# Kernel tuning notes

Hardware: AMD Instinct MI355X
Metric: run time of the kernel (lower is better)

The kernel has to match this reference:

```python
import jax, jax.numpy as jnp
import numpy as np

V, D, H, T, L, B = 32000, 1024, 16, 1024, 2, 2
HD = D // H
FF = 4 * D
EPS_RMS = 1.1920929e-07  # torch.finfo(float32).eps (RMSNorm default eps=None)
EPS_LN = 1e-5


def _rope_diag():
    # Faithful to the torch code: theta = 10000.0 ** (-2*i) // head_size
    # (** binds tighter than //), which is 0.0 for all i when head_size > 1,
    # and the einsum 'bimm,bim->bim' only reads the diagonal of the rotation
    # matrix, whose entries are cos((c+1)*theta).
    k = np.arange(0, HD, 2, dtype=np.float64)
    theta = (10000.0 ** (-2.0 * k)) // HD          # [HD//2], all zeros
    pos = np.arange(1, T + 1, dtype=np.float64)[:, None]
    cosv = np.cos(pos * theta)                      # [T, HD//2]
    diag = np.repeat(cosv, 2, axis=1)               # [T, HD]
    return jnp.asarray(diag, dtype=jnp.float32)


def setup_inputs() -> dict:
    key = jax.random.key(0)
    ks = jax.random.split(key, 12)
    s = 0.02
    n = lambda k, shape: jax.random.normal(k, shape, jnp.float32) * s
    return dict(
        idx=jax.random.randint(ks[0], (B, T), 0, V),
        emb=n(ks[1], (V, D)),
        wq=n(ks[2], (L, H, D, HD)),
        wk=n(ks[3], (L, H, D, HD)),
        wv=n(ks[4], (L, H, D, HD)),
        attn_w=n(ks[5], (L, D, D)),
        attn_b=jnp.zeros((L, D), jnp.float32),
        n1_w=jnp.ones((L, D), jnp.float32),
        n2_w=jnp.ones((L, D), jnp.float32),
        f1_w=n(ks[6], (L, D, FF)),
        f1_b=jnp.zeros((L, FF), jnp.float32),
        fs_w=n(ks[7], (L, FF, FF)),
        fs_b=jnp.zeros((L, FF), jnp.float32),
        f2_w=n(ks[8], (L, FF, D)),
        f2_b=jnp.zeros((L, D), jnp.float32),
        ln_w=jnp.ones((D,), jnp.float32),
        ln_b=jnp.zeros((D,), jnp.float32),
        out_w=n(ks[9], (D, V)),
        out_b=jnp.zeros((V,), jnp.float32),
    )


def _rmsnorm(x, w):
    return x * jax.lax.rsqrt(jnp.mean(x * x, axis=-1, keepdims=True) + EPS_RMS) * w


def _layernorm(x, w, b):
    mu = jnp.mean(x, axis=-1, keepdims=True)
    var = jnp.mean((x - mu) ** 2, axis=-1, keepdims=True)
    return (x - mu) * jax.lax.rsqrt(var + EPS_LN) * w + b


def _forward(idx, emb, wq, wk, wv, attn_w, attn_b, n1_w, n2_w,
             f1_w, f1_b, fs_w, fs_b, f2_w, f2_b, ln_w, ln_b, out_w, out_b):
    rope = _rope_diag()                              # [T, HD]
    mask = jnp.tril(jnp.ones((T, T), dtype=bool))    # causal
    scale = 1.0 / np.sqrt(HD)
    x = emb[idx]                                     # [B, T, D]
    for l in range(L):
        h = _rmsnorm(x, n1_w[l])
        q = jnp.einsum('btd,hdk->bhtk', h, wq[l])
        k = jnp.einsum('btd,hdk->bhtk', h, wk[l]) * rope[None, None]
        v = jnp.einsum('btd,hdk->bhtk', h, wv[l])
        score = jnp.einsum('bhtk,bhsk->bhts', q, k) * scale
        score = jnp.where(mask, score, -jnp.inf)
        att = jax.nn.softmax(score, axis=-1)
        o = jnp.einsum('bhts,bhsk->bhtk', att, v)
        o = o.transpose(0, 2, 1, 3).reshape(B, T, D)  # concat heads
        x = x + (o @ attn_w[l] + attn_b[l])
        h = _rmsnorm(x, n2_w[l])
        a = h @ f1_w[l] + f1_b[l]
        g = a @ fs_w[l] + fs_b[l]                     # fcswiglu applied to fc1 output
        x = x + (jax.nn.silu(a) * g) @ f2_w[l] + f2_b[l]
    x = _layernorm(x, ln_w, ln_b)
    return x @ out_w + out_b                          # [B, T, V]


def reference(idx, emb, wq, wk, wv, attn_w, attn_b, n1_w, n2_w,
              f1_w, f1_b, fs_w, fs_b, f2_w, f2_b, ln_w, ln_b, out_w, out_b):
    return _forward(idx, emb, wq, wk, wv, attn_w, attn_b, n1_w, n2_w,
                    f1_w, f1_b, fs_w, fs_b, f2_w, f2_b, ln_w, ln_b, out_w, out_b)
```

## Files before the change

### kernel.cpp

```cpp
#include <hip/hip_runtime.h>

#define BB   2
#define TT   1024
#define HH   16
#define DD   1024
#define HDD  64
#define FFD  4096
#define VV   32000
#define LLAY 2

typedef __bf16 bf16x8 __attribute__((ext_vector_type(8)));
typedef float  f32x4  __attribute__((ext_vector_type(4)));
typedef unsigned short u16x8 __attribute__((ext_vector_type(8)));

__device__ __forceinline__ float bf2f(ushort u) {
    return __uint_as_float(((unsigned int)u) << 16);
}
__device__ __forceinline__ ushort f2bf(float f) {
    unsigned int u = __float_as_uint(f);
    u += 0x7fffu + ((u >> 16) & 1u);
    return (ushort)(u >> 16);
}

__device__ __forceinline__ void gl_lds16(const ushort* g, ushort* l) {
    typedef const __attribute__((address_space(1))) unsigned int* gp_t;
    typedef __attribute__((address_space(3))) unsigned int* lp_t;
    __builtin_amdgcn_global_load_lds((gp_t)g, (lp_t)l, 16, 0, 0);
}

__global__ void embed_k(const int* __restrict__ idx, const float* __restrict__ emb,
                        float* __restrict__ x) {
    int row = blockIdx.x, tid = threadIdx.x;
    int e = idx[row];
    float4 f = *(const float4*)(emb + (size_t)e * DD + tid * 4);
    *(float4*)(x + (size_t)row * DD + tid * 4) = f;
}

__global__ __launch_bounds__(256) void rmsnorm_k(const float* __restrict__ x,
                                                 const float* __restrict__ w,
                                                 ushort* __restrict__ h) {
    int row = blockIdx.x, tid = threadIdx.x;
    int wave = tid >> 6, lane = tid & 63;
    const float* xr = x + (size_t)row * DD;
    float4 xv = *(const float4*)(xr + tid * 4);
    float s = xv.x * xv.x + xv.y * xv.y + xv.z * xv.z + xv.w * xv.w;
    for (int off = 32; off; off >>= 1) s += __shfl_xor(s, off, 64);
    __shared__ float red[4];
    if (lane == 0) red[wave] = s;
    __syncthreads();
    float tot = red[0] + red[1] + red[2] + red[3];
    float rs = rsqrtf(tot * (1.0f / DD) + 1.1920929e-07f);
    float4 wv = *(const float4*)(w + tid * 4);
    ushort4 hv;
    hv.x = f2bf(xv.x * rs * wv.x);
    hv.y = f2bf(xv.y * rs * wv.y);
    hv.z = f2bf(xv.z * rs * wv.z);
    hv.w = f2bf(xv.w * rs * wv.w);
    *(ushort4*)(h + (size_t)row * DD + tid * 4) = hv;
}

__global__ __launch_bounds__(256) void lnorm_k(const float* __restrict__ x,
                                               const float* __restrict__ w,
                                               const float* __restrict__ b,
                                               ushort* __restrict__ h) {
    int row = blockIdx.x, tid = threadIdx.x;
    int wave = tid >> 6, lane = tid & 63;
    const float* xr = x + (size_t)row * DD;
    float4 xv = *(const float4*)(xr + tid * 4);
    float s1 = xv.x + xv.y + xv.z + xv.w;
    for (int off = 32; off; off >>= 1) s1 += __shfl_xor(s1, off, 64);
    __shared__ float r1[4], r2[4];
    if (lane == 0) r1[wave] = s1;
    __syncthreads();
    float mu = (r1[0] + r1[1] + r1[2] + r1[3]) * (1.0f / DD);
    float dx0 = xv.x - mu, dx1 = xv.y - mu, dx2 = xv.z - mu, dx3 = xv.w - mu;
    float s2 = dx0 * dx0 + dx1 * dx1 + dx2 * dx2 + dx3 * dx3;
    for (int off = 32; off; off >>= 1) s2 += __shfl_xor(s2, off, 64);
    if (lane == 0) r2[wave] = s2;
    __syncthreads();
    float var = (r2[0] + r2[1] + r2[2] + r2[3]) * (1.0f / DD);
    float rs = rsqrtf(var + 1e-5f);
    float4 wv = *(const float4*)(w + tid * 4);
    float4 bv = *(const float4*)(b + tid * 4);
    ushort4 hv;
    hv.x = f2bf(dx0 * rs * wv.x + bv.x);
    hv.y = f2bf(dx1 * rs * wv.y + bv.y);
    hv.z = f2bf(dx2 * rs * wv.z + bv.z);
    hv.w = f2bf(dx3 * rs * wv.w + bv.w);
    *(ushort4*)(h + (size_t)row * DD + tid * 4) = hv;
}

__global__ void silu_k(ushort* __restrict__ a, const ushort* __restrict__ g) {
    int i = (blockIdx.x * 256 + threadIdx.x) * 4;
    ushort4 av = *(const ushort4*)(a + i);
    ushort4 gv = *(const ushort4*)(g + i);
    ushort4 ov;
    {
        float x = bf2f(av.x); ov.x = f2bf(x / (1.0f + __expf(-x)) * bf2f(gv.x));
        float y = bf2f(av.y); ov.y = f2bf(y / (1.0f + __expf(-y)) * bf2f(gv.y));
        float z = bf2f(av.z); ov.z = f2bf(z / (1.0f + __expf(-z)) * bf2f(gv.z));
        float u = bf2f(av.w); ov.w = f2bf(u / (1.0f + __expf(-u)) * bf2f(gv.w));
    }
    *(ushort4*)(a + i) = ov;
}

__global__ __launch_bounds__(256) void transp_k(const float* __restrict__ in,
                                                ushort* __restrict__ out,
                                                int K, int N,
                                                long long inB, long long outB) {
    __shared__ int tbuf[64][65];
    const float* ip = in + (size_t)blockIdx.z * inB;
    ushort* op = out + (size_t)blockIdx.z * outB;
    int n0 = blockIdx.x * 64, k0 = blockIdx.y * 64;
    int tid = threadIdx.x;
#pragma unroll
    for (int jj = 0; jj < 4; ++jj) {
        int idxq = tid + jj * 256;
        int rr = idxq >> 4;
        int cc = (idxq & 15) * 4;
        float4 f = *(const float4*)(ip + (size_t)(k0 + rr) * N + n0 + cc);
        tbuf[rr][cc]     = f2bf(f.x);
        tbuf[rr][cc + 1] = f2bf(f.y);
        tbuf[rr][cc + 2] = f2bf(f.z);
        tbuf[rr][cc + 3] = f2bf(f.w);
    }
    __syncthreads();
#pragma unroll
    for (int jj = 0; jj < 4; ++jj) {
        int idxq = tid + jj * 256;
        int rr = idxq >> 4;
        int cc = (idxq & 15) * 4;
        ushort4 v;
        v.x = (ushort)tbuf[cc][rr];
        v.y = (ushort)tbuf[cc + 1][rr];
        v.z = (ushort)tbuf[cc + 2][rr];
        v.w = (ushort)tbuf[cc + 3][rr];
        *(ushort4*)(op + (size_t)(n0 + rr) * K + k0 + cc) = v;
    }
}

template <bool BIAS, bool RESID, bool OUTBF>
__global__ __launch_bounds__(256) void gemm_k(const ushort* __restrict__ A,
                                              const ushort* __restrict__ Bt,
                                              const float* __restrict__ bias,
                                              const float* __restrict__ resid,
                                              void* __restrict__ Cout,
                                              int M, int N, int K) {
    __shared__ __align__(16) ushort As[2][128 * 32];
    __shared__ __align__(16) ushort Bs[2][128 * 32];
    const int tid = threadIdx.x;
    const int m0 = blockIdx.y * 128, n0 = blockIdx.x * 128;
    const int wave = tid >> 6, lane = tid & 63;
    const int waveM = (wave >> 1) * 64, waveN = (wave & 1) * 64;
    const int lrow = lane & 15, quad = lane >> 4;

    const int srow = wave * 32 + (lane >> 2);
    const int scol = (lane & 3) * 8;
    const ushort* pa = A + (size_t)(m0 + srow) * K + scol;
    const ushort* pb = Bt + (size_t)(n0 + srow) * K + scol;
    ushort* lA = &As[0][0] + wave * 32 * 32;
    ushort* lB = &Bs[0][0] + wave * 32 * 32;

    f32x4 acc[4][4];
    f32x4 zero = {0.f, 0.f, 0.f, 0.f};
#pragma unroll
    for (int i = 0; i < 4; i++)
#pragma unroll
        for (int j = 0; j < 4; j++) acc[i][j] = zero;

    const int nk = K >> 5;

#define STAGE(buf, kt)                                                         \
    do {                                                                       \
        const ushort* ga = pa + (size_t)(kt) * 32;                             \
        const ushort* gb = pb + (size_t)(kt) * 32;                             \
        ushort* la = lA + (size_t)(buf) * 128 * 32;                            \
        ushort* lb = lB + (size_t)(buf) * 128 * 32;                            \
        gl_lds16(ga, la);                                                      \
        gl_lds16(ga + (size_t)16 * K, la + 16 * 32);                           \
        gl_lds16(gb, lb);                                                      \
        gl_lds16(gb + (size_t)16 * K, lb + 16 * 32);                           \
    } while (0)

    STAGE(0, 0);
    int cur = 0;
    for (int kt = 0; kt < nk; ++kt) {
        __syncthreads();
        if (kt + 1 < nk) STAGE(cur ^ 1, kt + 1);
        bf16x8 af[4], bfr[4];
#pragma unroll
        for (int i = 0; i < 4; i++)
            af[i] = *(const bf16x8*)&As[cur][(waveM + i * 16 + lrow) * 32 + quad * 8];
#pragma unroll
        for (int j = 0; j < 4; j++)
            bfr[j] = *(const bf16x8*)&Bs[cur][(waveN + j * 16 + lrow) * 32 + quad * 8];
#pragma unroll
        for (int i = 0; i < 4; i++)
#pragma unroll
            for (int j = 0; j < 4; j++)
                acc[i][j] = __builtin_amdgcn_mfma_f32_16x16x32_bf16(af[i], bfr[j], acc[i][j], 0, 0, 0);
        cur ^= 1;
    }
#undef STAGE

#pragma unroll
    for (int i = 0; i < 4; i++) {
#pragma unroll
        for (int j = 0; j < 4; j++) {
            int colg = n0 + waveN + j * 16 + lrow;
            float bv = BIAS ? bias[colg] : 0.f;
#pragma unroll
            for (int rr = 0; rr < 4; ++rr) {
                int rowg = m0 + waveM + i * 16 + quad * 4 + rr;
                size_t off = (size_t)rowg * N + colg;
                float vv = acc[i][j][rr] + bv;
                if (RESID) vv += resid[off];
                if (OUTBF) ((ushort*)Cout)[off] = f2bf(vv);
                else       ((float*)Cout)[off] = vv;
            }
        }
    }
}

__global__ __launch_bounds__(128) void attn_k(const ushort* __restrict__ qkv,
                                              ushort* __restrict__ o) {
    __shared__ __align__(16) ushort vt[64 * 80];
    __shared__ __align__(16) ushort pl[2 * 16 * 80];
    const int bid = blockIdx.x;
    const int bh = bid & 31;
    const int qt = 31 - (bid >> 5);
    const int b = bh >> 4, h = bh & 15;
    const int t0 = qt * 32;
    const int tid = threadIdx.x, wave = tid >> 6, lane = tid & 63;
    const int lrow = lane & 15, quad = lane >> 4;
    const int LD3 = 3 * DD;
    const size_t base3 = (size_t)(b * TT) * LD3 + (size_t)h * HDD;
    const int t0w = t0 + wave * 16;

    const ushort* qrow = qkv + base3 + (size_t)(t0w + lrow) * LD3 + quad * 8;
    bf16x8 af0 = *(const bf16x8*)(qrow);
    bf16x8 af1 = *(const bf16x8*)(qrow + 32);

    f32x4 acc_o[4];
    f32x4 zero = {0.f, 0.f, 0.f, 0.f};
#pragma unroll
    for (int n = 0; n < 4; ++n) acc_o[n] = zero;
    float m_r[4], l_r[4];
#pragma unroll
    for (int r = 0; r < 4; ++r) { m_r[r] = -1e30f; l_r[r] = 0.f; }

    ushort* plw = pl + wave * 16 * 80;

    const int smax = t0 + 31;
    for (int s0 = 0; s0 <= smax; s0 += 64) {
        __syncthreads();
        bf16x8 bk[4][2];
#pragma unroll
        for (int j = 0; j < 4; ++j) {
            const ushort* kr = qkv + base3 + (size_t)(s0 + j * 16 + lrow) * LD3 + DD + quad * 8;
            bk[j][0] = *(const bf16x8*)(kr);
            bk[j][1] = *(const bf16x8*)(kr + 32);
        }
#pragma unroll
        for (int cc = 0; cc < 4; ++cc) {
            int qch = tid + cc * 128;
            int s = qch & 63, d0 = (qch >> 6) * 8;
            u16x8 vv = *(const u16x8*)(qkv + base3 + (size_t)(s0 + s) * LD3 + 2 * DD + d0);
#pragma unroll
            for (int i = 0; i < 8; ++i) vt[(d0 + i) * 80 + s] = vv[i];
        }
        f32x4 accs[4];
#pragma unroll
        for (int j = 0; j < 4; ++j) {
            accs[j] = zero;
            accs[j] = __builtin_amdgcn_mfma_f32_16x16x32_bf16(af0, bk[j][0], accs[j], 0, 0, 0);
            accs[j] = __builtin_amdgcn_mfma_f32_16x16x32_bf16(af1, bk[j][1], accs[j], 0, 0, 0);
        }
        float pv[4][4];
#pragma unroll
        for (int r = 0; r < 4; ++r) {
            int qg = t0w + quad * 4 + r;
            float scv[4], tmax = -1e30f;
#pragma unroll
            for (int j = 0; j < 4; ++j) {
                int sg = s0 + j * 16 + lrow;
                float sc = (sg <= qg) ? accs[j][r] * 0.125f : -1e30f;
                scv[j] = sc;
                tmax = fmaxf(tmax, sc);
            }
            tmax = fmaxf(tmax, __shfl_xor(tmax, 1, 64));
            tmax = fmaxf(tmax, __shfl_xor(tmax, 2, 64));
            tmax = fmaxf(tmax, __shfl_xor(tmax, 4, 64));
            tmax = fmaxf(tmax, __shfl_xor(tmax, 8, 64));
            float mn = fmaxf(m_r[r], tmax);
            float ps = 0.f;
#pragma unroll
            for (int j = 0; j < 4; ++j) {
                float p = __expf(scv[j] - mn);
                pv[j][r] = p;
                ps += p;
            }
            ps += __shfl_xor(ps, 1, 64);
            ps += __shfl_xor(ps, 2, 64);
            ps += __shfl_xor(ps, 4, 64);
            ps += __shfl_xor(ps, 8, 64);
            float alpha = __expf(m_r[r] - mn);
            l_r[r] = l_r[r] * alpha + ps;
            m_r[r] = mn;
#pragma unroll
            for (int n = 0; n < 4; ++n) acc_o[n][r] *= alpha;
        }
#pragma unroll
        for (int j = 0; j < 4; ++j)
#pragma unroll
            for (int r = 0; r < 4; ++r)
                plw[(quad * 4 + r) * 80 + j * 16 + lrow] = f2bf(pv[j][r]);
        __syncthreads();
        bf16x8 pa0 = *(const bf16x8*)&plw[lrow * 80 + quad * 8];
        bf16x8 pa1 = *(const bf16x8*)&plw[lrow * 80 + 32 + quad * 8];
#pragma unroll
        for (int n = 0; n < 4; ++n) {
            bf16x8 bv0 = *(const bf16x8*)&vt[(n * 16 + lrow) * 80 + quad * 8];
            bf16x8 bv1 = *(const bf16x8*)&vt[(n * 16 + lrow) * 80 + 32 + quad * 8];
            acc_o[n] = __builtin_amdgcn_mfma_f32_16x16x32_bf16(pa0, bv0, acc_o[n], 0, 0, 0);
            acc_o[n] = __builtin_amdgcn_mfma_f32_16x16x32_bf16(pa1, bv1, acc_o[n], 0, 0, 0);
        }
    }
#pragma unroll
    for (int n = 0; n < 4; ++n)
#pragma unroll
        for (int r = 0; r < 4; ++r) {
            int tg = t0w + quad * 4 + r;
            o[(size_t)(b * TT + tg) * DD + h * HDD + n * 16 + lrow] = f2bf(acc_o[n][r] / l_r[r]);
        }
}

extern "C" void kernel_launch(void* const* d_in, const int* in_sizes, int n_in,
                              void* d_out, int out_size, void* d_ws, size_t ws_size,
                              hipStream_t stream) {
    const int*   idx    = (const int*)d_in[0];
    const float* emb    = (const float*)d_in[1];
    const float* wq     = (const float*)d_in[2];
    const float* wk     = (const float*)d_in[3];
    const float* wvv    = (const float*)d_in[4];
    const float* attn_w = (const float*)d_in[5];
    const float* attn_b = (const float*)d_in[6];
    const float* n1_w   = (const float*)d_in[7];
    const float* n2_w   = (const float*)d_in[8];
    const float* f1_w   = (const float*)d_in[9];
    const float* f1_b   = (const float*)d_in[10];
    const float* fs_w   = (const float*)d_in[11];
    const float* fs_b   = (const float*)d_in[12];
    const float* f2_w   = (const float*)d_in[13];
    const float* f2_b   = (const float*)d_in[14];
    const float* ln_w   = (const float*)d_in[15];
    const float* ln_b   = (const float*)d_in[16];
    const float* out_w  = (const float*)d_in[17];
    const float* out_b  = (const float*)d_in[18];

    const int BT = BB * TT;

    char* ws = (char*)d_ws;
    size_t off = 0;
    float* x = (float*)(ws + off);          off += (size_t)BT * DD * 4;
    ushort* wpack = (ushort*)(ws + off);    off += (size_t)VV * DD * 2;
    ushort* h = (ushort*)(ws + off);        off += (size_t)BT * DD * 2;
    ushort* qkv = (ushort*)(ws + off);      off += (size_t)BT * 3 * DD * 2;
    ushort* ob = (ushort*)(ws + off);       off += (size_t)BT * DD * 2;
    ushort* a = (ushort*)(ws + off);        off += (size_t)BT * FFD * 2;
    ushort* g = (ushort*)(ws + off);        off += (size_t)BT * FFD * 2;

    ushort* qkvT = wpack;
    ushort* attnT = wpack + (size_t)3 * DD * DD;
    ushort* f1T  = attnT + (size_t)DD * DD;
    ushort* fsT  = f1T + (size_t)FFD * DD;
    ushort* f2T  = fsT + (size_t)FFD * FFD;

    dim3 blk(256);

    embed_k<<<BT, blk, 0, stream>>>(idx, emb, x);

    for (int l = 0; l < LLAY; ++l) {
        const size_t woff_qkv = (size_t)l * HH * DD * HDD;
        transp_k<<<dim3(1, 16, 16), blk, 0, stream>>>(wq + woff_qkv, qkvT, DD, HDD,
                                                      (long long)DD * HDD, (long long)HDD * DD);
        transp_k<<<dim3(1, 16, 16), blk, 0, stream>>>(wk + woff_qkv, qkvT + (size_t)DD * DD, DD, HDD,
                                                      (long long)DD * HDD, (long long)HDD * DD);
        transp_k<<<dim3(1, 16, 16), blk, 0, stream>>>(wvv + woff_qkv, qkvT + (size_t)2 * DD * DD, DD, HDD,
                                                      (long long)DD * HDD, (long long)HDD * DD);
        transp_k<<<dim3(16, 16, 1), blk, 0, stream>>>(attn_w + (size_t)l * DD * DD, attnT, DD, DD, 0, 0);
        transp_k<<<dim3(64, 16, 1), blk, 0, stream>>>(f1_w + (size_t)l * DD * FFD, f1T, DD, FFD, 0, 0);
        transp_k<<<dim3(64, 64, 1), blk, 0, stream>>>(fs_w + (size_t)l * FFD * FFD, fsT, FFD, FFD, 0, 0);
        transp_k<<<dim3(16, 64, 1), blk, 0, stream>>>(f2_w + (size_t)l * FFD * DD, f2T, FFD, DD, 0, 0);

        rmsnorm_k<<<BT, blk, 0, stream>>>(x, n1_w + l * DD, h);
        gemm_k<false, false, true><<<dim3(24, 16), blk, 0, stream>>>(h, qkvT, nullptr, nullptr, qkv,
                                                                     BT, 3 * DD, DD);
        attn_k<<<BB * HH * (TT / 32), dim3(128), 0, stream>>>(qkv, ob);
        gemm_k<true, true, false><<<dim3(8, 16), blk, 0, stream>>>(ob, attnT, attn_b + l * DD, x, x,
                                                                   BT, DD, DD);
        rmsnorm_k<<<BT, blk, 0, stream>>>(x, n2_w + l * DD, h);
        gemm_k<true, false, true><<<dim3(32, 16), blk, 0, stream>>>(h, f1T, f1_b + l * FFD, nullptr, a,
                                                                    BT, FFD, DD);
        gemm_k<true, false, true><<<dim3(32, 16), blk, 0, stream>>>(a, fsT, fs_b + l * FFD, nullptr, g,
                                                                    BT, FFD, FFD);
        silu_k<<<(BT * FFD) / 1024, blk, 0, stream>>>(a, g);
        gemm_k<true, true, false><<<dim3(8, 16), blk, 0, stream>>>(a, f2T, f2_b + l * DD, x, x,
                                                                   BT, DD, FFD);
    }

    lnorm_k<<<BT, blk, 0, stream>>>(x, ln_w, ln_b, h);
    transp_k<<<dim3(500, 16, 1), blk, 0, stream>>>(out_w, wpack, DD, VV, 0, 0);
    gemm_k<true, false, false><<<dim3(250, 16), blk, 0, stream>>>(h, wpack, out_b, nullptr,
                                                                  (float*)d_out, BT, VV, DD);
}
```

Before: 1.408 ms.

## Triple-buffer GEMM loads, fuse SiLU gate into fs GEMM epilogue, nontemporal logits

The GEMM k-loop moves from double to triple buffering in LDS. It waits with explicit vmcnt counts and a single barrier per iteration, so global-to-LDS loads run two tiles ahead of the MFMA work. The standalone SiLU kernel is removed and silu(a)*g is computed in the epilogue of the fcswiglu GEMM, reading a as an auxiliary input. The final logits GEMM writes its fp32 output with nontemporal stores. The costs are more LDS per block, which may lower occupancy, and the hand-written waitcnt/barrier logic, which depends on the exact number of outstanding loads.

```diff
diff --git a/kernel.cpp b/kernel.cpp
--- a/kernel.cpp
+++ b/kernel.cpp
@@ -90,20 +90,6 @@
     *(ushort4*)(h + (size_t)row * DD + tid * 4) = hv;
 }
 
-__global__ void silu_k(ushort* __restrict__ a, const ushort* __restrict__ g) {
-    int i = (blockIdx.x * 256 + threadIdx.x) * 4;
-    ushort4 av = *(const ushort4*)(a + i);
-    ushort4 gv = *(const ushort4*)(g + i);
-    ushort4 ov;
-    {
-        float x = bf2f(av.x); ov.x = f2bf(x / (1.0f + __expf(-x)) * bf2f(gv.x));
-        float y = bf2f(av.y); ov.y = f2bf(y / (1.0f + __expf(-y)) * bf2f(gv.y));
-        float z = bf2f(av.z); ov.z = f2bf(z / (1.0f + __expf(-z)) * bf2f(gv.z));
-        float u = bf2f(av.w); ov.w = f2bf(u / (1.0f + __expf(-u)) * bf2f(gv.w));
-    }
-    *(ushort4*)(a + i) = ov;
-}
-
 __global__ __launch_bounds__(256) void transp_k(const float* __restrict__ in,
                                                 ushort* __restrict__ out,
                                                 int K, int N,
@@ -139,15 +125,15 @@
     }
 }
 
-template <bool BIAS, bool RESID, bool OUTBF>
+template <bool BIAS, int EPI, bool OUTBF, bool NT>
 __global__ __launch_bounds__(256) void gemm_k(const ushort* __restrict__ A,
                                               const ushort* __restrict__ Bt,
                                               const float* __restrict__ bias,
-                                              const float* __restrict__ resid,
+                                              const void* __restrict__ aux,
                                               void* __restrict__ Cout,
                                               int M, int N, int K) {
-    __shared__ __align__(16) ushort As[2][128 * 32];
-    __shared__ __align__(16) ushort Bs[2][128 * 32];
+    __shared__ __align__(16) ushort As[3][128 * 32];
+    __shared__ __align__(16) ushort Bs[3][128 * 32];
     const int tid = threadIdx.x;
     const int m0 = blockIdx.y * 128, n0 = blockIdx.x * 128;
     const int wave = tid >> 6, lane = tid & 63;
@@ -183,23 +169,26 @@
     } while (0)
 
     STAGE(0, 0);
-    int cur = 0;
+    if (nk > 1) STAGE(1, 1);
     for (int kt = 0; kt < nk; ++kt) {
-        __syncthreads();
-        if (kt + 1 < nk) STAGE(cur ^ 1, kt + 1);
+        if (kt + 1 < nk) asm volatile("s_waitcnt vmcnt(4)" ::: "memory");
+        else             asm volatile("s_waitcnt vmcnt(0)" ::: "memory");
+        __builtin_amdgcn_s_barrier();
+        __builtin_amdgcn_sched_barrier(0);
+        if (kt + 2 < nk) STAGE((kt + 2) % 3, kt + 2);
+        const int sl = kt % 3;
         bf16x8 af[4], bfr[4];
 #pragma unroll
         for (int i = 0; i < 4; i++)
-            af[i] = *(const bf16x8*)&As[cur][(waveM + i * 16 + lrow) * 32 + quad * 8];
+            af[i] = *(const bf16x8*)&As[sl][(waveM + i * 16 + lrow) * 32 + quad * 8];
 #pragma unroll
         for (int j = 0; j < 4; j++)
-            bfr[j] = *(const bf16x8*)&Bs[cur][(waveN + j * 16 + lrow) * 32 + quad * 8];
+            bfr[j] = *(const bf16x8*)&Bs[sl][(waveN + j * 16 + lrow) * 32 + quad * 8];
 #pragma unroll
         for (int i = 0; i < 4; i++)
 #pragma unroll
             for (int j = 0; j < 4; j++)
                 acc[i][j] = __builtin_amdgcn_mfma_f32_16x16x32_bf16(af[i], bfr[j], acc[i][j], 0, 0, 0);
-        cur ^= 1;
     }
 #undef STAGE
 
@@ -214,9 +203,14 @@
                 int rowg = m0 + waveM + i * 16 + quad * 4 + rr;
                 size_t off = (size_t)rowg * N + colg;
                 float vv = acc[i][j][rr] + bv;
-                if (RESID) vv += resid[off];
+                if (EPI == 1) vv += ((const float*)aux)[off];
+                if (EPI == 2) {
+                    float s = bf2f(((const ushort*)aux)[off]);
+                    vv *= s / (1.0f + __expf(-s));
+                }
                 if (OUTBF) ((ushort*)Cout)[off] = f2bf(vv);
-                else       ((float*)Cout)[off] = vv;
+                else if (NT) __builtin_nontemporal_store(vv, (float*)Cout + off);
+                else ((float*)Cout)[off] = vv;
             }
         }
     }
@@ -394,23 +388,22 @@
         transp_k<<<dim3(16, 64, 1), blk, 0, stream>>>(f2_w + (size_t)l * FFD * DD, f2T, FFD, DD, 0, 0);
 
         rmsnorm_k<<<BT, blk, 0, stream>>>(x, n1_w + l * DD, h);
-        gemm_k<false, false, true><<<dim3(24, 16), blk, 0, stream>>>(h, qkvT, nullptr, nullptr, qkv,
-                                                                     BT, 3 * DD, DD);
+        gemm_k<false, 0, true, false><<<dim3(24, 16), blk, 0, stream>>>(h, qkvT, nullptr, nullptr, qkv,
+                                                                        BT, 3 * DD, DD);
         attn_k<<<BB * HH * (TT / 32), dim3(128), 0, stream>>>(qkv, ob);
-        gemm_k<true, true, false><<<dim3(8, 16), blk, 0, stream>>>(ob, attnT, attn_b + l * DD, x, x,
-                                                                   BT, DD, DD);
+        gemm_k<true, 1, false, false><<<dim3(8, 16), blk, 0, stream>>>(ob, attnT, attn_b + l * DD, x, x,
+                                                                       BT, DD, DD);
         rmsnorm_k<<<BT, blk, 0, stream>>>(x, n2_w + l * DD, h);
-        gemm_k<true, false, true><<<dim3(32, 16), blk, 0, stream>>>(h, f1T, f1_b + l * FFD, nullptr, a,
-                                                                    BT, FFD, DD);
-        gemm_k<true, false, true><<<dim3(32, 16), blk, 0, stream>>>(a, fsT, fs_b + l * FFD, nullptr, g,
-                                                                    BT, FFD, FFD);
-        silu_k<<<(BT * FFD) / 1024, blk, 0, stream>>>(a, g);
-        gemm_k<true, true, false><<<dim3(8, 16), blk, 0, stream>>>(a, f2T, f2_b + l * DD, x, x,
-                                                                   BT, DD, FFD);
+        gemm_k<true, 0, true, false><<<dim3(32, 16), blk, 0, stream>>>(h, f1T, f1_b + l * FFD, nullptr, a,
+                                                                       BT, FFD, DD);
+        gemm_k<true, 2, true, false><<<dim3(32, 16), blk, 0, stream>>>(a, fsT, fs_b + l * FFD, a, g,
+                                                                       BT, FFD, FFD);
+        gemm_k<true, 1, false, false><<<dim3(8, 16), blk, 0, stream>>>(g, f2T, f2_b + l * DD, x, x,
+                                                                       BT, DD, FFD);
     }
 
     lnorm_k<<<BT, blk, 0, stream>>>(x, ln_w, ln_b, h);
     transp_k<<<dim3(500, 16, 1), blk, 0, stream>>>(out_w, wpack, DD, VV, 0, 0);
-    gemm_k<true, false, false><<<dim3(250, 16), blk, 0, stream>>>(h, wpack, out_b, nullptr,
-                                                                  (float*)d_out, BT, VV, DD);
-}
+    gemm_k<true, 0, false, true><<<dim3(250, 16), blk, 0, stream>>>(h, wpack, out_b, nullptr,
+                                                                    (float*)d_out, BT, VV, DD);
+}
```

Result: no change. 1.430 ms (+1.6%).
